# Optimization experiments

Measured on AMD Instinct MI355X. Metric: run time of the kernel, lower is better.

Reference implementation:

```python
import jax, jax.numpy as jnp
import numpy as np

P = 8  # patch size (hardcoded in unfold/fold of the original module)


def conv2d(x, w, b, groups=1):
    # x: (N,C,H,W), w: (O, C//groups, 3, 3), 'SAME' padding = padding=1 for 3x3
    y = jax.lax.conv_general_dilated(
        x, w, window_strides=(1, 1), padding='SAME',
        dimension_numbers=('NCHW', 'OIHW', 'NCHW'),
        feature_group_count=groups)
    return y + b[None, :, None, None]


def unfold8(x):
    # F.unfold(kernel=8, stride=8): (N,C,H,W) -> (N, C*64, L), channel-major then
    # kernel-row/col ordering, patches in row-major order.
    N, C, H, W = x.shape
    x = x.reshape(N, C, H // P, P, W // P, P)
    x = x.transpose(0, 1, 3, 5, 2, 4)        # N,C,ki,kj,nh,nw
    return x.reshape(N, C * P * P, (H // P) * (W // P))


def fold8(x, H, W):
    # inverse of unfold8 (non-overlapping, stride == kernel)
    N = x.shape[0]
    C = x.shape[1] // (P * P)
    x = x.reshape(N, C, P, P, H // P, W // P)
    x = x.transpose(0, 1, 4, 2, 5, 3)        # N,C,nh,ki,nw,kj
    return x.reshape(N, C, H, W)


def setup_inputs() -> dict:
    key = jax.random.key(0)
    ks = jax.random.split(key, 9)
    c = 64
    x = jax.random.normal(ks[0], (16, 7, c, 64, 64), dtype=jnp.float32)
    wq = jax.random.normal(ks[1], (c, 1, 3, 3), dtype=jnp.float32) * 0.05
    wk = jax.random.normal(ks[2], (c, 1, 3, 3), dtype=jnp.float32) * 0.05
    wv = jax.random.normal(ks[3], (c, c, 3, 3), dtype=jnp.float32) * 0.05
    wc = jax.random.normal(ks[4], (c, c, 3, 3), dtype=jnp.float32) * 0.05
    bq = jnp.zeros((c,), jnp.float32)
    bk = jnp.zeros((c,), jnp.float32)
    bv = jnp.zeros((c,), jnp.float32)
    bc = jnp.zeros((c,), jnp.float32)
    return {"x": x, "wq": wq, "bq": bq, "wk": wk, "bk": bk,
            "wv": wv, "bv": bv, "wc": wc, "bc": bc}


def reference(x, wq, bq, wk, bk, wv, bv, wc, bc):
    heads = 1
    b, t, c, h, w = x.shape
    D = P * P * c          # dim
    d = D // heads         # hidden_dim per head
    L = (h // P) * (w // P)  # num patches per frame

    xf = x.reshape(-1, c, h, w)
    q = unfold8(conv2d(xf, wq, bq, groups=c))   # depthwise conv
    k = unfold8(conv2d(xf, wk, bk, groups=c))   # depthwise conv
    v = unfold8(conv2d(xf, wv, bv))             # dense conv

    def rearr(u):
        # (b*t, D, L) -> (b, heads, d, t*L)
        return u.reshape(b, t, heads, d, L).transpose(0, 2, 3, 1, 4).reshape(b, heads, d, t * L)

    q, k, v = rearr(q), rearr(k), rearr(v)

    attn = jnp.einsum('bhds,bhdu->bhsu', q, k) * (d ** -0.5)  # (b,H,tL,tL)
    attn = jax.nn.softmax(attn, axis=-1)
    out = jnp.einsum('bhsu,bhdu->bhsd', attn, v)               # (b,H,tL,d)

    out = out.reshape(b, heads, t, L, d).transpose(0, 2, 1, 4, 3).reshape(b * t, D, L)
    feat = fold8(out, h, w)
    return conv2d(feat, wc, bc).reshape(x.shape) + x
```

## Files before the change

### kernel.cpp

```cpp
#include <hip/hip_runtime.h>
#include <hip/hip_bf16.h>


namespace {
constexpr int NFR = 112;
constexpr int T_  = 7;
constexpr int B_  = 16;
constexpr int C_  = 64;
constexpr int H_  = 64;
constexpr int W_  = 64;
constexpr int S_  = 448;
constexpr int D_  = 4096;
constexpr size_t QKV_E = (size_t)B_ * S_ * D_;
constexpr size_t ATTN_E = (size_t)B_ * S_ * S_;
}

typedef __attribute__((ext_vector_type(8))) short short8v;
typedef __attribute__((ext_vector_type(4))) float float4v;

__device__ __forceinline__ float bfu2f(unsigned short u) {
    union { unsigned int i; float f; } v; v.i = ((unsigned int)u) << 16; return v.f;
}
__device__ __forceinline__ unsigned short f2bf(float f) {
    __hip_bfloat16 h = __float2bfloat16(f);
    return *reinterpret_cast<unsigned short*>(&h);
}

__device__ __forceinline__ short8v frag_ld(const char* ldsb, int r, int kByte) {
    return *(const short8v*)(ldsb + r * 128 + (kByte ^ ((r & 7) << 4)));
}

template<int NTHR>
__device__ __forceinline__ void stage_tile(char* ldsb, const unsigned short* g,
                                           int ldg, int t) {
    #pragma unroll
    for (int i = 0; i < 1024 / NTHR; ++i) {
        int e = i * NTHR + t;
        int r = e >> 3, c8 = (e & 7) * 8;
        short8v v = *(const short8v*)(g + (size_t)r * ldg + c8);
        *(short8v*)(ldsb + r * 128 + ((c8 * 2) ^ ((r & 7) << 4))) = v;
    }
}

__device__ __forceinline__ void stage_vt(char* ldsb, const unsigned short* g, int t) {
    int d0 = (t & 15) * 8;
    int u0 = (t >> 4) * 4;
    short8v r0 = *(const short8v*)(g + (size_t)(u0 + 0) * D_ + d0);
    short8v r1 = *(const short8v*)(g + (size_t)(u0 + 1) * D_ + d0);
    short8v r2 = *(const short8v*)(g + (size_t)(u0 + 2) * D_ + d0);
    short8v r3 = *(const short8v*)(g + (size_t)(u0 + 3) * D_ + d0);
    #pragma unroll
    for (int j = 0; j < 8; ++j) {
        unsigned int lo = (unsigned short)r0[j] | (((unsigned int)(unsigned short)r1[j]) << 16);
        unsigned int hi = (unsigned short)r2[j] | (((unsigned int)(unsigned short)r3[j]) << 16);
        int d = d0 + j;
        int byte = d * 128 + (((unsigned)(u0 * 2)) ^ ((d & 7) << 4));
        *(uint2*)(ldsb + byte) = uint2{lo, hi};
    }
}

__global__ __launch_bounds__(256) void prep_w2(const float* __restrict__ wv,
                                               const float* __restrict__ wc,
                                               __hip_bfloat16* __restrict__ Wt_v,
                                               __hip_bfloat16* __restrict__ Wt_c)
{
    int t = blockIdx.x * 256 + threadIdx.x;
    if (t >= 2 * 36864) return;
    int which = t >= 36864;
    int i = t - which * 36864;
    const float* s = which ? wc : wv;
    __hip_bfloat16* d = which ? Wt_c : Wt_v;
    int r = i >> 12, co = (i >> 6) & 63, ci = i & 63;
    d[i] = __float2bfloat16(s[(co * 64 + ci) * 9 + r]);
}

template<bool IS_V>
__global__ __launch_bounds__(512, 4) void conv_mfma6(
    const void* __restrict__ src,
    const __hip_bfloat16* __restrict__ Wt,
    const float* __restrict__ bias,
    const float* __restrict__ xin,
    void* __restrict__ dst,
    const float* __restrict__ wq, const float* __restrict__ bq,
    const float* __restrict__ wk, const float* __restrict__ bk,
    unsigned short* __restrict__ Qout, unsigned short* __restrict__ Kout)
{
    __shared__ char xs[6 * 66 * 128];
    __shared__ char wl[2][64 * 128];
    __shared__ float wqk_s[IS_V ? 1280 : 1];
    const int f    = blockIdx.y;
    const int band = blockIdx.x;
    const int y0   = band * 4;
    const int tid  = threadIdx.x;
    const int lane = tid & 63;
    const int w    = tid >> 6;
    const int q    = lane >> 4;
    const int l15  = lane & 15;
    const int wrow = w >> 1;
    const int wco  = w & 1;

    const unsigned short* Wg = (const unsigned short*)Wt;
    const int r0w = tid >> 3, c0w = (tid & 7) * 8;
    const int wlo = r0w * 128 + ((c0w * 2) ^ ((r0w & 7) << 4));
    const unsigned short* wgl = Wg + r0w * 64 + c0w;

    short8v w0A = *(const short8v*)(wgl);

    if constexpr (IS_V) {
        for (int e = tid; e < 1280; e += 512) {
            float v;
            if (e < 576)       v = wq[e];
            else if (e < 1152) v = wk[e - 576];
            else if (e < 1216) v = bq[e - 1152];
            else               v = bk[e - 1216];
            wqk_s[e] = v;
        }
    }

    for (int e = tid; e < 6 * 16 * 64; e += 512) {
        int x  = e & 63;
        int cg = (e >> 6) & 15;
        int r  = e >> 10;
        int y  = y0 - 1 + r;
        unsigned short p[4];
        if ((unsigned)y < (unsigned)H_) {
            #pragma unroll
            for (int j = 0; j < 4; ++j) {
                size_t gi = (((size_t)f * C_ + cg * 4 + j) * H_ + y) * W_ + x;
                if constexpr (IS_V) p[j] = f2bf(((const float*)src)[gi]);
                else                p[j] = ((const unsigned short*)src)[gi];
            }
        } else { p[0] = p[1] = p[2] = p[3] = 0; }
        int xp = x + 1;
        int byte = (r * 66 + xp) * 128 + ((cg * 8) ^ ((xp & 7) << 4));
        *(uint2*)(xs + byte) = *(uint2*)p;
    }
    for (int e = tid; e < 6 * 16 * 2; e += 512) {
        int side = e & 1;
        int cg   = (e >> 1) & 15;
        int r    = e >> 5;
        int xp   = side ? 65 : 0;
        int byte = (r * 66 + xp) * 128 + ((cg * 8) ^ ((xp & 7) << 4));
        *(uint2*)(xs + byte) = uint2{0u, 0u};
    }
    *(short8v*)(wl[0] + wlo) = w0A;
    __syncthreads();

    float4v acc[4][2] = {};
    #pragma unroll
    for (int tap = 0; tap < 9; ++tap) {
        const int ky = tap / 3, kx = tap - ky * 3;
        short8v nwA;
        if (tap + 1 < 9) {
            nwA = *(const short8v*)(wgl + (tap + 1) * 4096);
            __builtin_amdgcn_sched_barrier(0);
        }
        const char* wb = wl[tap & 1];
        const int ri = wrow + ky;
        #pragma unroll
        for (int kc = 0; kc < 2; ++kc) {
            int kB = kc * 64 + q * 16;
            short8v bfr[2];
            #pragma unroll
            for (int nt = 0; nt < 2; ++nt)
                bfr[nt] = frag_ld(wb, wco * 32 + nt * 16 + l15, kB);
            #pragma unroll
            for (int xt = 0; xt < 4; ++xt) {
                int xp = xt * 16 + l15 + kx;
                short8v av = *(const short8v*)(xs + (ri * 66 + xp) * 128 +
                                               (kB ^ ((xp & 7) << 4)));
                #pragma unroll
                for (int nt = 0; nt < 2; ++nt)
                    acc[xt][nt] = __builtin_amdgcn_mfma_f32_16x16x32_bf16(
                        av, bfr[nt], acc[xt][nt], 0, 0, 0);
            }
        }
        if (tap + 1 < 9) {
            *(short8v*)(wl[(tap + 1) & 1] + wlo) = nwA;
        }
        __syncthreads();
    }

    float bco[2];
    #pragma unroll
    for (int nt = 0; nt < 2; ++nt) bco[nt] = bias[wco * 32 + nt * 16 + l15];
    const int bb = f / T_, tt = f % T_;
    const int R = y0 + wrow;
    #pragma unroll
    for (int xt = 0; xt < 4; ++xt) {
        #pragma unroll
        for (int nt = 0; nt < 2; ++nt) {
            int co = wco * 32 + nt * 16 + l15;
            if constexpr (IS_V) {
                int s  = tt * 64 + (R >> 3) * 8 + xt * 2 + (q >> 1);
                int d0 = co * 64 + (R & 7) * 8 + (q & 1) * 4;
                unsigned short pk[4];
                #pragma unroll
                for (int j = 0; j < 4; ++j)
                    pk[j] = f2bf(acc[xt][nt][j] + bco[nt]);
                *(uint2*)((unsigned short*)dst + ((size_t)bb * S_ + s) * D_ + d0) =
                    *(const uint2*)pk;
            } else {
                size_t o = (((size_t)f * C_ + co) * H_ + R) * W_ + xt * 16 + q * 4;
                float4 rv = *(const float4*)(xin + o);
                float4 ov;
                ov.x = acc[xt][nt][0] + bco[nt] + rv.x;
                ov.y = acc[xt][nt][1] + bco[nt] + rv.y;
                ov.z = acc[xt][nt][2] + bco[nt] + rv.z;
                ov.w = acc[xt][nt][3] + bco[nt] + rv.w;
                *(float4*)((float*)dst + o) = ov;
            }
        }
    }

    if constexpr (IS_V) {
        const int c4 = lane >> 2;
        const int r2 = lane & 3;
        const int px = w;
        const int cb = c4 * 4;
        const int yk = ((band & 1) << 2) + r2;
        const int s  = tt * 64 + (band >> 1) * 8 + px;
        float acq[4][8], ack[4][8];
        #pragma unroll
        for (int i = 0; i < 4; ++i) {
            float bqv = wqk_s[1152 + cb + i];
            float bkv = wqk_s[1216 + cb + i];
            #pragma unroll
            for (int j = 0; j < 8; ++j) { acq[i][j] = bqv; ack[i][j] = bkv; }
        }
        #pragma unroll
        for (int dy = 0; dy < 3; ++dy) {
            const int ri = r2 + dy;
            float wq4[3][4], wk4[3][4];
            #pragma unroll
            for (int kx = 0; kx < 3; ++kx)
                #pragma unroll
                for (int i = 0; i < 4; ++i) {
                    wq4[kx][i] = wqk_s[(cb + i) * 9 + dy * 3 + kx];
                    wk4[kx][i] = wqk_s[576 + (cb + i) * 9 + dy * 3 + kx];
                }
            #pragma unroll
            for (int u = 0; u < 10; ++u) {
                int xp = px * 8 + u;
                int byte = (ri * 66 + xp) * 128 + ((cb * 2) ^ ((xp & 7) << 4));
                uint2 pr = *(const uint2*)(xs + byte);
                float rv[4];
                rv[0] = bfu2f((unsigned short)(pr.x & 0xffffu));
                rv[1] = bfu2f((unsigned short)(pr.x >> 16));
                rv[2] = bfu2f((unsigned short)(pr.y & 0xffffu));
                rv[3] = bfu2f((unsigned short)(pr.y >> 16));
                #pragma unroll
                for (int kx = 0; kx < 3; ++kx) {
                    const int j = u - kx;
                    if (j >= 0 && j < 8) {
                        #pragma unroll
                        for (int i = 0; i < 4; ++i) {
                            acq[i][j] += wq4[kx][i] * rv[i];
                            ack[i][j] += wk4[kx][i] * rv[i];
                        }
                    }
                }
            }
        }
        #pragma unroll
        for (int i = 0; i < 4; ++i) {
            unsigned short pq[8], pk[8];
            #pragma unroll
            for (int j = 0; j < 8; ++j) {
                pq[j] = f2bf(acq[i][j]);
                pk[j] = f2bf(ack[i][j]);
            }
            size_t off = ((size_t)bb * S_ + s) * D_ + (size_t)(cb + i) * 64 + yk * 8;
            *(short8v*)(Qout + off) = *(const short8v*)pq;
            *(short8v*)(Kout + off) = *(const short8v*)pk;
        }
    }
}

__global__ __launch_bounds__(1024, 4) void gemm_qk_mfma(
    const __hip_bfloat16* __restrict__ Qg,
    const __hip_bfloat16* __restrict__ Kg,
    float* __restrict__ ATTN)
{
    __shared__ alignas(16) char lds[65536];
    const int tid = threadIdx.x;
    const int kh  = tid >> 9;
    const int t   = tid & 511;
    char* ldsA = lds + kh * 32768;
    char* ldsB = ldsA + 16384;
    int bid = blockIdx.x;
    int lb  = (bid & 7) * 32 + (bid >> 3);
    int bb  = lb >> 4;
    int m0  = ((lb >> 2) & 3) * 128;
    int n0  = (lb & 3) * 128;
    const unsigned short* Ag = (const unsigned short*)Qg + (size_t)bb * S_ * D_
                               + (size_t)m0 * D_ + kh * 2048;
    const unsigned short* Bg = (const unsigned short*)Kg + (size_t)bb * S_ * D_
                               + (size_t)n0 * D_ + kh * 2048;
    int w = t >> 6, l = t & 63, q = l >> 4, l15 = l & 15;
    int wm = w >> 2, wn = w & 3;
    int r0 = t >> 3, c0 = (t & 7) * 8;
    int r1 = 64 + r0;
    short8v sA0, sA1, sB0, sB1;
    sA0 = *(const short8v*)(Ag + (size_t)r0 * D_ + c0);
    sA1 = *(const short8v*)(Ag + (size_t)r1 * D_ + c0);
    sB0 = *(const short8v*)(Bg + (size_t)r0 * D_ + c0);
    sB1 = *(const short8v*)(Bg + (size_t)r1 * D_ + c0);

    float4v acc[4][2] = {};
    int swz0 = (c0 * 2) ^ ((r0 & 7) << 4);
    for (int k0 = 0; k0 < 2048; k0 += 64) {
        __syncthreads();
        *(short8v*)(ldsA + r0 * 128 + swz0) = sA0;
        *(short8v*)(ldsA + r1 * 128 + swz0) = sA1;
        *(short8v*)(ldsB + r0 * 128 + swz0) = sB0;
        *(short8v*)(ldsB + r1 * 128 + swz0) = sB1;
        if (k0 + 64 < 2048) {
            int kn = k0 + 64;
            sA0 = *(const short8v*)(Ag + (size_t)r0 * D_ + kn + c0);
            sA1 = *(const short8v*)(Ag + (size_t)r1 * D_ + kn + c0);
            sB0 = *(const short8v*)(Bg + (size_t)r0 * D_ + kn + c0);
            sB1 = *(const short8v*)(Bg + (size_t)r1 * D_ + kn + c0);
        }
        __syncthreads();
        #pragma unroll
        for (int kc = 0; kc < 2; ++kc) {
            int kB = kc * 64 + q * 16;
            short8v a[4], b[2];
            #pragma unroll
            for (int mt = 0; mt < 4; ++mt) a[mt] = frag_ld(ldsA, wm * 64 + mt * 16 + l15, kB);
            #pragma unroll
            for (int nt = 0; nt < 2; ++nt) b[nt] = frag_ld(ldsB, wn * 32 + nt * 16 + l15, kB);
            #pragma unroll
            for (int mt = 0; mt < 4; ++mt)
                #pragma unroll
                for (int nt = 0; nt < 2; ++nt)
                    acc[mt][nt] = __builtin_amdgcn_mfma_f32_16x16x32_bf16(
                        a[mt], b[nt], acc[mt][nt], 0, 0, 0);
        }
    }

    __syncthreads();
    if (kh) {
        #pragma unroll
        for (int mt = 0; mt < 4; ++mt)
            #pragma unroll
            for (int nt = 0; nt < 2; ++nt)
                *(float4v*)(lds + (mt * 2 + nt) * 8192 + t * 16) = acc[mt][nt];
    }
    __syncthreads();
    if (!kh) {
        const float scale = 1.0f / 64.0f;
        #pragma unroll
        for (int mt = 0; mt < 4; ++mt) {
            #pragma unroll
            for (int nt = 0; nt < 2; ++nt) {
                float4v o = *(const float4v*)(lds + (mt * 2 + nt) * 8192 + t * 16);
                float4v v = acc[mt][nt];
                int u = n0 + wn * 32 + nt * 16 + l15;
                #pragma unroll
                for (int j = 0; j < 4; ++j) {
                    int s = m0 + wm * 64 + mt * 16 + q * 4 + j;
                    if (s < S_ && u < S_)
                        ATTN[((size_t)bb * S_ + s) * S_ + u] = (v[j] + o[j]) * scale;
                }
            }
        }
    }
}

__global__ __launch_bounds__(64) void softmax_rows(const float* __restrict__ ATTN,
                                                   unsigned short* __restrict__ P)
{
    size_t row = blockIdx.x;
    const float* p = ATTN + row * S_;
    int lane = threadIdx.x;
    float vals[7];
    float m = -1e30f;
    #pragma unroll
    for (int i = 0; i < 7; ++i) { vals[i] = p[lane + i * 64]; m = fmaxf(m, vals[i]); }
    #pragma unroll
    for (int off = 32; off; off >>= 1) m = fmaxf(m, __shfl_xor(m, off));
    float sum = 0.f;
    #pragma unroll
    for (int i = 0; i < 7; ++i) { vals[i] = __expf(vals[i] - m); sum += vals[i]; }
    #pragma unroll
    for (int off = 32; off; off >>= 1) sum += __shfl_xor(sum, off);
    float inv = 1.f / sum;
    #pragma unroll
    for (int i = 0; i < 7; ++i) P[row * S_ + lane + i * 64] = f2bf(vals[i] * inv);
}

__global__ __launch_bounds__(256, 2) void gemm_pv_mfma(
    const unsigned short* __restrict__ Pg,
    const __hip_bfloat16* __restrict__ Vg,
    __hip_bfloat16* __restrict__ FEAT)
{
    __shared__ alignas(16) char lds[32768];
    char* ldsA = lds;
    char* ldsB = lds + 16384;
    int bid = blockIdx.x;
    int lb  = (bid & 7) * 256 + (bid >> 3);
    int bb  = lb >> 7;
    int tl  = lb & 127;
    int m0  = (tl >> 5) * 128;
    int n0  = (tl & 31) * 128;
    const unsigned short* Ag = Pg + (size_t)bb * S_ * S_ + (size_t)m0 * S_;
    const unsigned short* Bg = (const unsigned short*)Vg + (size_t)bb * S_ * D_ + n0;
    int t = threadIdx.x;
    int w = t >> 6, l = t & 63, q = l >> 4, l15 = l & 15;
    int wm = w >> 1, wn = w & 1;
    float4v acc[4][4] = {};
    for (int k0 = 0; k0 < S_; k0 += 64) {
        __syncthreads();
        stage_tile<256>(ldsA, Ag + k0, S_, t);
        stage_vt(ldsB, Bg + (size_t)k0 * D_, t);
        __syncthreads();
        #pragma unroll
        for (int kc = 0; kc < 2; ++kc) {
            int kB = kc * 64 + q * 16;
            short8v a[4], b[4];
            #pragma unroll
            for (int mt = 0; mt < 4; ++mt) a[mt] = frag_ld(ldsA, wm * 64 + mt * 16 + l15, kB);
            #pragma unroll
            for (int nt = 0; nt < 4; ++nt) b[nt] = frag_ld(ldsB, wn * 64 + nt * 16 + l15, kB);
            #pragma unroll
            for (int mt = 0; mt < 4; ++mt)
                #pragma unroll
                for (int nt = 0; nt < 4; ++nt)
                    acc[mt][nt] = __builtin_amdgcn_mfma_f32_16x16x32_bf16(
                        a[mt], b[nt], acc[mt][nt], 0, 0, 0);
        }
    }
    #pragma unroll
    for (int mt = 0; mt < 4; ++mt) {
        #pragma unroll
        for (int j = 0; j < 4; ++j) {
            int s = m0 + wm * 64 + mt * 16 + q * 4 + j;
            if (s >= S_) continue;
            int f  = bb * T_ + (s >> 6);
            int l6 = s & 63;
            #pragma unroll
            for (int nt = 0; nt < 4; ++nt) {
                int d = n0 + wn * 64 + nt * 16 + l15;
                int c = d >> 6, r = d & 63;
                int y  = ((l6 >> 3) << 3) + (r >> 3);
                int xx = ((l6 & 7) << 3) + (r & 7);
                FEAT[(((size_t)f * C_ + c) * H_ + y) * W_ + xx] =
                    __float2bfloat16(acc[mt][nt][j]);
            }
        }
    }
}

extern "C" void kernel_launch(void* const* d_in, const int* in_sizes, int n_in,
                              void* d_out, int out_size, void* d_ws, size_t ws_size,
                              hipStream_t stream)
{
    const float* x  = (const float*)d_in[0];
    const float* wq = (const float*)d_in[1];
    const float* bq = (const float*)d_in[2];
    const float* wk = (const float*)d_in[3];
    const float* bk = (const float*)d_in[4];
    const float* wv = (const float*)d_in[5];
    const float* bv = (const float*)d_in[6];
    const float* wc = (const float*)d_in[7];
    const float* bc = (const float*)d_in[8];
    float* out = (float*)d_out;

    __hip_bfloat16* Qb = (__hip_bfloat16*)d_ws;
    __hip_bfloat16* Kb = Qb + QKV_E;
    __hip_bfloat16* Vb = Kb + QKV_E;
    float* ATTN = (float*)(Vb + QKV_E);
    __hip_bfloat16* Wt_v = (__hip_bfloat16*)(ATTN + ATTN_E);
    __hip_bfloat16* Wt_c = Wt_v + 9 * 64 * 64;
    unsigned short* Pb   = (unsigned short*)Kb;
    __hip_bfloat16* FEAT = Qb;

    prep_w2<<<288, 256, 0, stream>>>(wv, wc, Wt_v, Wt_c);

    conv_mfma6<true><<<dim3(16, NFR), 512, 0, stream>>>(
        x, Wt_v, bv, nullptr, Vb,
        wq, bq, wk, bk, (unsigned short*)Qb, (unsigned short*)Kb);
    gemm_qk_mfma<<<256, 1024, 0, stream>>>(Qb, Kb, ATTN);
    softmax_rows<<<B_ * S_, 64, 0, stream>>>(ATTN, Pb);
    gemm_pv_mfma<<<2048, 256, 0, stream>>>(Pb, Vb, FEAT);
    conv_mfma6<false><<<dim3(16, NFR), 512, 0, stream>>>(
        FEAT, Wt_c, bc, x, out,
        nullptr, nullptr, nullptr, nullptr, nullptr, nullptr);
}
```

Before: 337.7 us.

## Split conv tiles into half-width column blocks with extra LDS swizzle

The conv kernels now tile each frame into 4-row by 32-column blocks instead of full 64-wide bands, doubling the grid and halving LDS and accumulator usage so more blocks fit per CU (launch bounds raised to 6). The halo columns are now loaded from neighbouring pixels rather than zeroed, and an extra row-dependent XOR swizzle is added to LDS addressing to reduce bank conflicts. The depthwise Q/K part is remapped so each thread handles 2 channels. The cost is more halo reloading and more weight loads per output, in exchange for better occupancy and load balance.

```diff
diff --git a/kernel.cpp b/kernel.cpp
--- a/kernel.cpp
+++ b/kernel.cpp
@@ -75,7 +75,7 @@
 }
 
 template<bool IS_V>
-__global__ __launch_bounds__(512, 4) void conv_mfma6(
+__global__ __launch_bounds__(512, 6) void conv_mfma7(
     const void* __restrict__ src,
     const __hip_bfloat16* __restrict__ Wt,
     const float* __restrict__ bias,
@@ -85,19 +85,22 @@
     const float* __restrict__ wk, const float* __restrict__ bk,
     unsigned short* __restrict__ Qout, unsigned short* __restrict__ Kout)
 {
-    __shared__ char xs[6 * 66 * 128];
+    __shared__ char xs[6 * 34 * 128];
     __shared__ char wl[2][64 * 128];
     __shared__ float wqk_s[IS_V ? 1280 : 1];
-    const int f    = blockIdx.y;
-    const int band = blockIdx.x;
-    const int y0   = band * 4;
-    const int tid  = threadIdx.x;
-    const int lane = tid & 63;
-    const int w    = tid >> 6;
-    const int q    = lane >> 4;
-    const int l15  = lane & 15;
-    const int wrow = w >> 1;
-    const int wco  = w & 1;
+    const int f     = blockIdx.y;
+    const int bx    = blockIdx.x;
+    const int bandy = bx & 15;
+    const int bxh   = bx >> 4;
+    const int y0    = bandy * 4;
+    const int x0    = bxh * 32;
+    const int tid   = threadIdx.x;
+    const int lane  = tid & 63;
+    const int w     = tid >> 6;
+    const int q     = lane >> 4;
+    const int l15   = lane & 15;
+    const int wrow  = w >> 1;
+    const int wco   = w & 1;
 
     const unsigned short* Wg = (const unsigned short*)Wt;
     const int r0w = tid >> 3, c0w = (tid & 7) * 8;
@@ -117,36 +120,49 @@
         }
     }
 
-    for (int e = tid; e < 6 * 16 * 64; e += 512) {
-        int x  = e & 63;
-        int cg = (e >> 6) & 15;
-        int r  = e >> 10;
+    for (int e = tid; e < 3072; e += 512) {
+        int x  = e & 31;
+        int cg = (e >> 5) & 15;
+        int r  = e >> 9;
         int y  = y0 - 1 + r;
         unsigned short p[4];
         if ((unsigned)y < (unsigned)H_) {
             #pragma unroll
             for (int j = 0; j < 4; ++j) {
-                size_t gi = (((size_t)f * C_ + cg * 4 + j) * H_ + y) * W_ + x;
+                size_t gi = (((size_t)f * C_ + cg * 4 + j) * H_ + y) * W_ + x0 + x;
                 if constexpr (IS_V) p[j] = f2bf(((const float*)src)[gi]);
                 else                p[j] = ((const unsigned short*)src)[gi];
             }
         } else { p[0] = p[1] = p[2] = p[3] = 0; }
         int xp = x + 1;
-        int byte = (r * 66 + xp) * 128 + ((cg * 8) ^ ((xp & 7) << 4));
+        int byte = (r * 34 + xp) * 128 +
+                   ((cg * 8) ^ ((xp & 7) << 4) ^ ((r & 3) << 5));
         *(uint2*)(xs + byte) = *(uint2*)p;
     }
-    for (int e = tid; e < 6 * 16 * 2; e += 512) {
+    for (int e = tid; e < 192; e += 512) {
         int side = e & 1;
         int cg   = (e >> 1) & 15;
         int r    = e >> 5;
-        int xp   = side ? 65 : 0;
-        int byte = (r * 66 + xp) * 128 + ((cg * 8) ^ ((xp & 7) << 4));
-        *(uint2*)(xs + byte) = uint2{0u, 0u};
+        int y    = y0 - 1 + r;
+        int xg   = x0 + (side ? 32 : -1);
+        unsigned short p[4];
+        if ((unsigned)y < (unsigned)H_ && (unsigned)xg < (unsigned)W_) {
+            #pragma unroll
+            for (int j = 0; j < 4; ++j) {
+                size_t gi = (((size_t)f * C_ + cg * 4 + j) * H_ + y) * W_ + xg;
+                if constexpr (IS_V) p[j] = f2bf(((const float*)src)[gi]);
+                else                p[j] = ((const unsigned short*)src)[gi];
+            }
+        } else { p[0] = p[1] = p[2] = p[3] = 0; }
+        int xp = side ? 33 : 0;
+        int byte = (r * 34 + xp) * 128 +
+                   ((cg * 8) ^ ((xp & 7) << 4) ^ ((r & 3) << 5));
+        *(uint2*)(xs + byte) = *(uint2*)p;
     }
     *(short8v*)(wl[0] + wlo) = w0A;
     __syncthreads();
 
-    float4v acc[4][2] = {};
+    float4v acc[2][2] = {};
     #pragma unroll
     for (int tap = 0; tap < 9; ++tap) {
         const int ky = tap / 3, kx = tap - ky * 3;
@@ -157,6 +173,7 @@
         }
         const char* wb = wl[tap & 1];
         const int ri = wrow + ky;
+        const int rx = (ri & 3) << 5;
         #pragma unroll
         for (int kc = 0; kc < 2; ++kc) {
             int kB = kc * 64 + q * 16;
@@ -165,10 +182,10 @@
             for (int nt = 0; nt < 2; ++nt)
                 bfr[nt] = frag_ld(wb, wco * 32 + nt * 16 + l15, kB);
             #pragma unroll
-            for (int xt = 0; xt < 4; ++xt) {
+            for (int xt = 0; xt < 2; ++xt) {
                 int xp = xt * 16 + l15 + kx;
-                short8v av = *(const short8v*)(xs + (ri * 66 + xp) * 128 +
-                                               (kB ^ ((xp & 7) << 4)));
+                short8v av = *(const short8v*)(xs + (ri * 34 + xp) * 128 +
+                                               ((kB ^ ((xp & 7) << 4)) ^ rx));
                 #pragma unroll
                 for (int nt = 0; nt < 2; ++nt)
                     acc[xt][nt] = __builtin_amdgcn_mfma_f32_16x16x32_bf16(
@@ -187,12 +204,12 @@
     const int bb = f / T_, tt = f % T_;
     const int R = y0 + wrow;
     #pragma unroll
-    for (int xt = 0; xt < 4; ++xt) {
+    for (int xt = 0; xt < 2; ++xt) {
         #pragma unroll
         for (int nt = 0; nt < 2; ++nt) {
             int co = wco * 32 + nt * 16 + l15;
             if constexpr (IS_V) {
-                int s  = tt * 64 + (R >> 3) * 8 + xt * 2 + (q >> 1);
+                int s  = tt * 64 + (R >> 3) * 8 + bxh * 4 + xt * 2 + (q >> 1);
                 int d0 = co * 64 + (R & 7) * 8 + (q & 1) * 4;
                 unsigned short pk[4];
                 #pragma unroll
@@ -201,7 +218,7 @@
                 *(uint2*)((unsigned short*)dst + ((size_t)bb * S_ + s) * D_ + d0) =
                     *(const uint2*)pk;
             } else {
-                size_t o = (((size_t)f * C_ + co) * H_ + R) * W_ + xt * 16 + q * 4;
+                size_t o = (((size_t)f * C_ + co) * H_ + R) * W_ + x0 + xt * 16 + q * 4;
                 float4 rv = *(const float4*)(xin + o);
                 float4 ov;
                 ov.x = acc[xt][nt][0] + bco[nt] + rv.x;
@@ -214,15 +231,17 @@
     }
 
     if constexpr (IS_V) {
-        const int c4 = lane >> 2;
+        const int hi = w >> 2;
+        const int px = w & 3;
+        const int c2 = hi * 16 + (lane >> 2);
         const int r2 = lane & 3;
-        const int px = w;
-        const int cb = c4 * 4;
-        const int yk = ((band & 1) << 2) + r2;
-        const int s  = tt * 64 + (band >> 1) * 8 + px;
-        float acq[4][8], ack[4][8];
-        #pragma unroll
-        for (int i = 0; i < 4; ++i) {
+        const int cb = c2 * 2;
+        const int yk = ((bandy & 1) << 2) + r2;
+        const int s  = tt * 64 + (bandy >> 1) * 8 + bxh * 4 + px;
+        const int cByte = (c2 >> 1) * 8 + (c2 & 1) * 4;
+        float acq[2][8], ack[2][8];
+        #pragma unroll
+        for (int i = 0; i < 2; ++i) {
             float bqv = wqk_s[1152 + cb + i];
             float bkv = wqk_s[1216 + cb + i];
             #pragma unroll
@@ -231,39 +250,37 @@
         #pragma unroll
         for (int dy = 0; dy < 3; ++dy) {
             const int ri = r2 + dy;
-            float wq4[3][4], wk4[3][4];
+            const int rx = (ri & 3) << 5;
+            float wq2[3][2], wk2[3][2];
             #pragma unroll
             for (int kx = 0; kx < 3; ++kx)
                 #pragma unroll
-                for (int i = 0; i < 4; ++i) {
-                    wq4[kx][i] = wqk_s[(cb + i) * 9 + dy * 3 + kx];
-                    wk4[kx][i] = wqk_s[576 + (cb + i) * 9 + dy * 3 + kx];
+                for (int i = 0; i < 2; ++i) {
+                    wq2[kx][i] = wqk_s[(cb + i) * 9 + dy * 3 + kx];
+                    wk2[kx][i] = wqk_s[576 + (cb + i) * 9 + dy * 3 + kx];
                 }
             #pragma unroll
             for (int u = 0; u < 10; ++u) {
                 int xp = px * 8 + u;
-                int byte = (ri * 66 + xp) * 128 + ((cb * 2) ^ ((xp & 7) << 4));
-                uint2 pr = *(const uint2*)(xs + byte);
-                float rv[4];
-                rv[0] = bfu2f((unsigned short)(pr.x & 0xffffu));
-                rv[1] = bfu2f((unsigned short)(pr.x >> 16));
-                rv[2] = bfu2f((unsigned short)(pr.y & 0xffffu));
-                rv[3] = bfu2f((unsigned short)(pr.y >> 16));
+                int byte = (ri * 34 + xp) * 128 +
+                           ((cByte ^ ((xp & 7) << 4)) ^ rx);
+                unsigned int pr = *(const unsigned int*)(xs + byte);
+                float rv0 = bfu2f((unsigned short)(pr & 0xffffu));
+                float rv1 = bfu2f((unsigned short)(pr >> 16));
                 #pragma unroll
                 for (int kx = 0; kx < 3; ++kx) {
                     const int j = u - kx;
                     if (j >= 0 && j < 8) {
-                        #pragma unroll
-                        for (int i = 0; i < 4; ++i) {
-                            acq[i][j] += wq4[kx][i] * rv[i];
-                            ack[i][j] += wk4[kx][i] * rv[i];
-                        }
+                        acq[0][j] += wq2[kx][0] * rv0;
+                        acq[1][j] += wq2[kx][1] * rv1;
+                        ack[0][j] += wk2[kx][0] * rv0;
+                        ack[1][j] += wk2[kx][1] * rv1;
                     }
                 }
             }
         }
         #pragma unroll
-        for (int i = 0; i < 4; ++i) {
+        for (int i = 0; i < 2; ++i) {
             unsigned short pq[8], pk[8];
             #pragma unroll
             for (int j = 0; j < 8; ++j) {
@@ -479,13 +496,13 @@
 
     prep_w2<<<288, 256, 0, stream>>>(wv, wc, Wt_v, Wt_c);
 
-    conv_mfma6<true><<<dim3(16, NFR), 512, 0, stream>>>(
+    conv_mfma7<true><<<dim3(32, NFR), 512, 0, stream>>>(
         x, Wt_v, bv, nullptr, Vb,
         wq, bq, wk, bk, (unsigned short*)Qb, (unsigned short*)Kb);
     gemm_qk_mfma<<<256, 1024, 0, stream>>>(Qb, Kb, ATTN);
     softmax_rows<<<B_ * S_, 64, 0, stream>>>(ATTN, Pb);
     gemm_pv_mfma<<<2048, 256, 0, stream>>>(Pb, Vb, FEAT);
-    conv_mfma6<false><<<dim3(16, NFR), 512, 0, stream>>>(
+    conv_mfma7<false><<<dim3(32, NFR), 512, 0, stream>>>(
         FEAT, Wt_c, bc, x, out,
         nullptr, nullptr, nullptr, nullptr, nullptr, nullptr);
 }
```

After: 397.5 us. 1.18x slower.
